# Performance work log

Hardware: AMD Instinct MI355X
Metric: run time of the kernel (lower is better)

The kernel has to match this reference:

```python
import jax, jax.numpy as jnp
import numpy as np

N = 100000
D = 64
E = 1000000


def setup_inputs() -> dict:
    key = jax.random.key(0)
    k_x, k_e, k_w1, k_b1, k_w2, k_b2 = jax.random.split(key, 6)
    x = jax.random.normal(k_x, (N, D), dtype=jnp.float32)
    edge_index = jax.random.randint(k_e, (2, E), 0, N, dtype=jnp.int64)
    # nn.Linear(2D, D): weight [D, 2D], bias [D]
    lim1 = 1.0 / np.sqrt(2 * D)
    W1 = jax.random.uniform(k_w1, (D, 2 * D), dtype=jnp.float32, minval=-lim1, maxval=lim1)
    b1 = jax.random.uniform(k_b1, (D,), dtype=jnp.float32, minval=-lim1, maxval=lim1)
    # nn.Linear(D, 1): weight [1, D], bias [1]
    lim2 = 1.0 / np.sqrt(D)
    W2 = jax.random.uniform(k_w2, (1, D), dtype=jnp.float32, minval=-lim2, maxval=lim2)
    b2 = jax.random.uniform(k_b2, (1,), dtype=jnp.float32, minval=-lim2, maxval=lim2)
    return {"x": x, "edge_index": edge_index, "W1": W1, "b1": b1, "W2": W2, "b2": b2}


def reference(x, edge_index, W1, b1, W2, b2):
    src = edge_index[0]
    dst = edge_index[1]
    # [E, 2D] gathered edge features
    edge_features = jnp.concatenate([x[src], x[dst]], axis=1)
    h = jax.nn.relu(edge_features @ W1.T + b1)  # [E, D]
    out = h @ W2.T + b2                          # [E, 1]
    return out.squeeze(-1)                       # [E]
```

## Files before the change

kernel.cpp:

```cpp
#include <hip/hip_runtime.h>

#define NDIM 64
#define FDIM 128

typedef _Float16 half8  __attribute__((ext_vector_type(8)));
typedef _Float16 half4v __attribute__((ext_vector_type(4)));
typedef float    float4v __attribute__((ext_vector_type(4)));

__global__ __launch_bounds__(256) void prep_wcomb_kernel(
    const float* __restrict__ W1, _Float16* __restrict__ Wcomb)
{
    int i = blockIdx.x * blockDim.x + threadIdx.x;
    if (i >= FDIM * NDIM) return;
    int j = i >> 6;
    int k = i & 63;
    float v = (j < NDIM) ? W1[j * FDIM + k] : W1[(j - NDIM) * FDIM + NDIM + k];
    Wcomb[i] = (_Float16)v;
}

__global__ __launch_bounds__(256) void node_gemm_kernel(
    const float* __restrict__ x,
    const _Float16* __restrict__ Wcomb,
    const float* __restrict__ b1,
    _Float16* __restrict__ Yab,
    int N)
{
    const int wave = threadIdx.x >> 6;
    const int lane = threadIdx.x & 63;
    const int c = lane & 15;
    const int g = lane >> 4;

    const int node0 = (blockIdx.x * 4 + wave) * 16;
    if (node0 >= N) return;

    half8 Bf[2];
    #pragma unroll
    for (int kk = 0; kk < 2; kk++) {
        const float* bp = x + (size_t)(node0 + c) * NDIM + kk * 32 + g * 8;
        float4v b0 = *(const float4v*)bp;
        float4v b1v_ = *(const float4v*)(bp + 4);
        half8 B;
        B[0] = (_Float16)b0[0]; B[1] = (_Float16)b0[1];
        B[2] = (_Float16)b0[2]; B[3] = (_Float16)b0[3];
        B[4] = (_Float16)b1v_[0]; B[5] = (_Float16)b1v_[1];
        B[6] = (_Float16)b1v_[2]; B[7] = (_Float16)b1v_[3];
        Bf[kk] = B;
    }

    float4v C[8];
    #pragma unroll
    for (int mt = 0; mt < 8; mt++) C[mt] = (float4v){0.f, 0.f, 0.f, 0.f};

    #pragma unroll
    for (int kk = 0; kk < 2; kk++) {
        #pragma unroll
        for (int mt = 0; mt < 8; mt++) {
            half8 Af = *(const half8*)(Wcomb + (size_t)(mt * 16 + c) * NDIM
                                       + kk * 32 + g * 8);
            C[mt] = __builtin_amdgcn_mfma_f32_16x16x32_f16(Af, Bf[kk], C[mt], 0, 0, 0);
        }
    }

    #pragma unroll
    for (int mt = 0; mt < 8; mt++) {
        float4v badd = (float4v){0.f, 0.f, 0.f, 0.f};
        if (mt < 4) badd = *(const float4v*)(b1 + mt * 16 + g * 4);
        half4v o;
        #pragma unroll
        for (int r = 0; r < 4; r++) o[r] = (_Float16)(C[mt][r] + badd[r]);
        *(half4v*)(Yab + (size_t)(node0 + c) * FDIM + mt * 16 + g * 4) = o;
    }
}

__global__ __launch_bounds__(256) void edge_combine_kernel(
    const _Float16* __restrict__ Yab,
    const int* __restrict__ ei,
    const float* __restrict__ W2,
    const float* __restrict__ b2,
    float* __restrict__ out,
    int E)
{
    const int lane = threadIdx.x & 63;
    const int wave = threadIdx.x >> 6;
    const int grp  = lane >> 3;
    const int j8   = lane & 7;

    const long e0 = (long)blockIdx.x * 256 + wave * 64;
    if (e0 >= E) return;

    float4v w2lo = *(const float4v*)(W2 + j8 * 8);
    float4v w2hi = *(const float4v*)(W2 + j8 * 8 + 4);
    const float b2v = b2[0];

    float keep = 0.f;
    #pragma unroll
    for (int t = 0; t < 8; t++) {
        const long e = e0 + t * 8 + grp;
        const int s = ei[e];
        const int d = ei[E + e];
        half8 a = *(const half8*)(Yab + (size_t)s * FDIM + j8 * 8);
        half8 b = *(const half8*)(Yab + (size_t)d * FDIM + 64 + j8 * 8);

        float acc = 0.f;
        #pragma unroll
        for (int u = 0; u < 8; u++) {
            float h = (float)a[u] + (float)b[u];
            h = h > 0.f ? h : 0.f;
            acc = fmaf(u < 4 ? w2lo[u] : w2hi[u - 4], h, acc);
        }
        acc += __shfl_xor(acc, 1, 64);
        acc += __shfl_xor(acc, 2, 64);
        acc += __shfl_xor(acc, 4, 64);
        if (j8 == t) keep = acc;
    }
    out[e0 + j8 * 8 + grp] = keep + b2v;
}

__global__ __launch_bounds__(256) void edge_mlp_fp32_kernel(
    const float* __restrict__ x, const int* __restrict__ ei,
    const float* __restrict__ W1, const float* __restrict__ b1,
    const float* __restrict__ W2, const float* __restrict__ b2,
    float* __restrict__ out, int E)
{
    int e = blockIdx.x * blockDim.x + threadIdx.x;
    if (e >= E) return;
    int s = ei[e];
    int d = ei[E + e];
    const float* xs = x + (size_t)s * NDIM;
    const float* xd = x + (size_t)d * NDIM;
    float acc = b2[0];
    for (int j = 0; j < NDIM; j++) {
        float h = b1[j];
        for (int k = 0; k < NDIM; k++) {
            h += xs[k] * W1[j * FDIM + k] + xd[k] * W1[j * FDIM + 64 + k];
        }
        acc += W2[j] * (h > 0.f ? h : 0.f);
    }
    out[e] = acc;
}

extern "C" void kernel_launch(void* const* d_in, const int* in_sizes, int n_in,
                              void* d_out, int out_size, void* d_ws, size_t ws_size,
                              hipStream_t stream) {
    const float* x  = (const float*)d_in[0];
    const int*   ei = (const int*)d_in[1];
    const float* W1 = (const float*)d_in[2];
    const float* b1 = (const float*)d_in[3];
    const float* W2 = (const float*)d_in[4];
    const float* b2 = (const float*)d_in[5];
    float* out = (float*)d_out;
    const int E = out_size;
    const int N = in_sizes[0] / NDIM;

    const size_t wcomb_bytes = (size_t)FDIM * NDIM * sizeof(_Float16);
    const size_t tbl_bytes   = (size_t)N * FDIM * sizeof(_Float16);

    if (ws_size >= wcomb_bytes + tbl_bytes && (N % 16) == 0 && (E % 64) == 0) {
        _Float16* Wcomb = (_Float16*)d_ws;
        _Float16* Yab   = (_Float16*)((char*)d_ws + wcomb_bytes);

        prep_wcomb_kernel<<<(FDIM * NDIM + 255) / 256, 256, 0, stream>>>(W1, Wcomb);

        const int nblocks = (N + 63) / 64;
        node_gemm_kernel<<<nblocks, 256, 0, stream>>>(x, Wcomb, b1, Yab, N);

        edge_combine_kernel<<<(E + 255) / 256, 256, 0, stream>>>(
            Yab, ei, W2, b2, out, E);
    } else {
        edge_mlp_fp32_kernel<<<(E + 255) / 256, 256, 0, stream>>>(
            x, ei, W1, b1, W2, b2, out, E);
    }
}
```

Before: 133.3 us.

## Compute edge W2 projection with MFMA and batch all gathers upfront

The edge combine kernel now maps each wave's 64 edges onto four 16x16x32 f16 MFMA tiles. Each tile does the add and ReLU in packed half precision and multiplies by a broadcast W2 fragment, replacing the per-lane FMA loop and the xor-shuffle reductions. All index loads and row gathers for the four tiles are issued before any compute, so more random memory requests are in flight at once. In exchange, the hidden activations are summed and clamped in fp16 rather than fp32, and the prefetched fragments raise register use.

Result: no change. 134.9 us (+1.2%).

```diff
diff --git a/kernel.cpp b/kernel.cpp
--- a/kernel.cpp
+++ b/kernel.cpp
@@ -82,38 +82,61 @@
 {
     const int lane = threadIdx.x & 63;
     const int wave = threadIdx.x >> 6;
-    const int grp  = lane >> 3;
-    const int j8   = lane & 7;
+    const int c = lane & 15;
+    const int g = lane >> 4;
 
-    const long e0 = (long)blockIdx.x * 256 + wave * 64;
+    const long e0 = (long)(blockIdx.x * 4 + wave) * 64;
     if (e0 >= E) return;
 
-    float4v w2lo = *(const float4v*)(W2 + j8 * 8);
-    float4v w2hi = *(const float4v*)(W2 + j8 * 8 + 4);
+    half8 Bw[2];
+    #pragma unroll
+    for (int kk = 0; kk < 2; kk++) {
+        const float* wp = W2 + kk * 32 + g * 8;
+        float4v w0 = *(const float4v*)wp;
+        float4v w1 = *(const float4v*)(wp + 4);
+        half8 B;
+        B[0] = (_Float16)w0[0]; B[1] = (_Float16)w0[1];
+        B[2] = (_Float16)w0[2]; B[3] = (_Float16)w0[3];
+        B[4] = (_Float16)w1[0]; B[5] = (_Float16)w1[1];
+        B[6] = (_Float16)w1[2]; B[7] = (_Float16)w1[3];
+        Bw[kk] = B;
+    }
     const float b2v = b2[0];
 
-    float keep = 0.f;
+    int s[4], d[4];
     #pragma unroll
-    for (int t = 0; t < 8; t++) {
-        const long e = e0 + t * 8 + grp;
-        const int s = ei[e];
-        const int d = ei[E + e];
-        half8 a = *(const half8*)(Yab + (size_t)s * FDIM + j8 * 8);
-        half8 b = *(const half8*)(Yab + (size_t)d * FDIM + 64 + j8 * 8);
+    for (int t = 0; t < 4; t++) {
+        s[t] = ei[e0 + t * 16 + c];
+        d[t] = ei[E + e0 + t * 16 + c];
+    }
 
-        float acc = 0.f;
+    half8 av[4][2], bv[4][2];
+    #pragma unroll
+    for (int t = 0; t < 4; t++) {
         #pragma unroll
-        for (int u = 0; u < 8; u++) {
-            float h = (float)a[u] + (float)b[u];
-            h = h > 0.f ? h : 0.f;
-            acc = fmaf(u < 4 ? w2lo[u] : w2hi[u - 4], h, acc);
+        for (int kk = 0; kk < 2; kk++) {
+            av[t][kk] = *(const half8*)(Yab + (size_t)s[t] * FDIM + kk * 32 + g * 8);
+            bv[t][kk] = *(const half8*)(Yab + (size_t)d[t] * FDIM + 64 + kk * 32 + g * 8);
         }
-        acc += __shfl_xor(acc, 1, 64);
-        acc += __shfl_xor(acc, 2, 64);
-        acc += __shfl_xor(acc, 4, 64);
-        if (j8 == t) keep = acc;
     }
-    out[e0 + j8 * 8 + grp] = keep + b2v;
+
+    const half8 zero8 = (half8)(_Float16)0.0f;
+    #pragma unroll
+    for (int t = 0; t < 4; t++) {
+        float4v C = (float4v){0.f, 0.f, 0.f, 0.f};
+        #pragma unroll
+        for (int kk = 0; kk < 2; kk++) {
+            half8 H = av[t][kk] + bv[t][kk];
+            H = __builtin_elementwise_max(H, zero8);
+            C = __builtin_amdgcn_mfma_f32_16x16x32_f16(H, Bw[kk], C, 0, 0, 0);
+        }
+        if (c == 0) {
+            float4v o;
+            #pragma unroll
+            for (int r = 0; r < 4; r++) o[r] = C[r] + b2v;
+            *(float4v*)(out + e0 + t * 16 + g * 4) = o;
+        }
+    }
 }
 
 __global__ __launch_bounds__(256) void edge_mlp_fp32_kernel(
@@ -164,7 +187,8 @@
         const int nblocks = (N + 63) / 64;
         node_gemm_kernel<<<nblocks, 256, 0, stream>>>(x, Wcomb, b1, Yab, N);
 
-        edge_combine_kernel<<<(E + 255) / 256, 256, 0, stream>>>(
+        const int eblocks = (E + 255) / 256;
+        edge_combine_kernel<<<eblocks, 256, 0, stream>>>(
             Yab, ei, W2, b2, out, E);
     } else {
         edge_mlp_fp32_kernel<<<(E + 255) / 256, 256, 0, stream>>>(
```
